# Kernel optimization log

Hardware: AMD Instinct MI355X
Metric: run time of the kernel (lower is better)

The kernel has to match this reference:

```python
import jax, jax.numpy as jnp
import numpy as np

B, H, W, C = 8, 128, 128, 256
NH = 8
HD = C // NH
WS = 8           # window size
SS = 4           # shift size
N = WS * WS      # tokens per window
SCALE = HD ** -0.5
EPS = 1e-5


def _rel_pos_index():
    coords = np.stack(np.meshgrid(np.arange(WS), np.arange(WS), indexing='ij'))  # [2,WS,WS]
    cf = coords.reshape(2, -1)                                                   # [2,N]
    rel = (cf[:, :, None] - cf[:, None, :]).transpose(1, 2, 0)                   # [N,N,2]
    rel[..., 0] += WS - 1
    rel[..., 1] += WS - 1
    rel[..., 0] *= 2 * WS - 1
    return rel.sum(-1)  # [N,N] indices into (2*WS-1)^2 table

RPI = jnp.asarray(_rel_pos_index())


def _attn_mask():
    img = np.zeros((H, W))
    slices = (slice(0, -WS), slice(-WS, -SS), slice(-SS, None))
    cnt = 0
    for hs in slices:
        for ws_ in slices:
            img[hs, ws_] = cnt
            cnt += 1
    mw = img.reshape(H // WS, WS, W // WS, WS).transpose(0, 2, 1, 3).reshape(-1, N)  # [nW,N]
    am = mw[:, None, :] - mw[:, :, None]
    return jnp.asarray(np.where(am != 0, -100.0, 0.0).astype(np.float32))  # [nW,N,N]

ATTN_MASK = _attn_mask()


def _ln(x, g, b):
    m = jnp.mean(x, -1, keepdims=True)
    v = jnp.var(x, -1, keepdims=True)
    return (x - m) * jax.lax.rsqrt(v + EPS) * g + b


def setup_inputs() -> dict:
    key = jax.random.key(0)
    ks = jax.random.split(key, 8)
    s = 0.02
    return {
        'x': jax.random.normal(ks[0], (B, H * W, C), jnp.float32),
        'qkv_w': jax.random.normal(ks[1], (C, 3 * C), jnp.float32) * s,
        'qkv_b': jnp.zeros((3 * C,), jnp.float32),
        'proj_w': jax.random.normal(ks[2], (C, C), jnp.float32) * s,
        'proj_b': jnp.zeros((C,), jnp.float32),
        'rpb': jax.random.normal(ks[3], ((2 * WS - 1) ** 2, NH), jnp.float32) * s,
        'g1': jnp.ones((C,), jnp.float32), 'b1': jnp.zeros((C,), jnp.float32),
        'g2': jnp.ones((C,), jnp.float32), 'b2': jnp.zeros((C,), jnp.float32),
        'fc1_w': jax.random.normal(ks[4], (C, 4 * C), jnp.float32) * s,
        'fc1_b': jnp.zeros((4 * C,), jnp.float32),
        'fc2_w': jax.random.normal(ks[5], (4 * C, C), jnp.float32) * s,
        'fc2_b': jnp.zeros((C,), jnp.float32),
    }


def reference(x, qkv_w, qkv_b, proj_w, proj_b, rpb, g1, b1, g2, b2,
              fc1_w, fc1_b, fc2_w, fc2_b):
    nW = (H // WS) * (W // WS)
    shortcut = x
    h = _ln(x, g1, b1).reshape(B, H, W, C)
    # cyclic shift
    h = jnp.roll(h, (-SS, -SS), axis=(1, 2))
    # window partition -> (B*nW, N, C)
    win = h.reshape(B, H // WS, WS, W // WS, WS, C).transpose(0, 1, 3, 2, 4, 5).reshape(-1, N, C)
    qkv = (win @ qkv_w + qkv_b).reshape(-1, N, 3, NH, HD).transpose(2, 0, 3, 1, 4)  # [3,B_,NH,N,HD]
    q, k, v = qkv[0] * SCALE, qkv[1], qkv[2]
    attn = jnp.einsum('bhnd,bhmd->bhnm', q, k)                    # [B_,NH,N,N]
    bias = rpb[RPI].transpose(2, 0, 1)                             # [NH,N,N]
    attn = attn + bias[None]
    attn = attn.reshape(B, nW, NH, N, N) + ATTN_MASK[None, :, None]
    attn = jax.nn.softmax(attn.reshape(-1, NH, N, N), axis=-1)
    out = jnp.einsum('bhnm,bhmd->bhnd', attn, v).transpose(0, 2, 1, 3).reshape(-1, N, C)
    out = out @ proj_w + proj_b
    # window reverse + reverse shift
    out = out.reshape(B, H // WS, W // WS, WS, WS, C).transpose(0, 1, 3, 2, 4, 5).reshape(B, H, W, C)
    out = jnp.roll(out, (SS, SS), axis=(1, 2)).reshape(B, H * W, C)
    x = shortcut + out
    hm = _ln(x, g2, b2)
    hm = jax.nn.gelu(hm @ fc1_w + fc1_b, approximate=False) @ fc2_w + fc2_b
    return x + hm
```

## Files before the change

kernel.cpp:

```cpp
#include <hip/hip_runtime.h>
#include <math.h>


#define NWIN_TOTAL 2048
#define TOK_TOTAL  131072
#define SCALE_Q    0.17677669529663687f
#define LOG2E      1.4426950408889634f

typedef unsigned short u16;
typedef __attribute__((ext_vector_type(4))) unsigned short u16x4;
typedef __attribute__((ext_vector_type(8))) unsigned short u16x8;
typedef __attribute__((ext_vector_type(8))) short bf16x8;
typedef __attribute__((ext_vector_type(4))) float f32x4;

#define AS1 __attribute__((address_space(1)))
#define AS3 __attribute__((address_space(3)))
#define GLOAD_LDS16(g, l) \
  __builtin_amdgcn_global_load_lds((const AS1 unsigned int*)(g), (AS3 unsigned int*)(l), 16, 0, 0)

__device__ __forceinline__ float bf2f(u16 u) {
  union { unsigned int i; float f; } c; c.i = ((unsigned int)u) << 16; return c.f;
}
__device__ __forceinline__ u16 f2bf(float f) {
  union { float f; unsigned int i; } c; c.f = f;
  return (u16)((c.i + 0x7fff + ((c.i >> 16) & 1)) >> 16);
}
__device__ __forceinline__ int regid3(int h) { return h < 120 ? 0 : (h < 124 ? 1 : 2); }
__device__ __forceinline__ float gelu_f(float v) {
  float t = exp2f(v * fmaf(v * v, 0.10294423f, 2.3022082f));
  return v * t * __builtin_amdgcn_rcpf(t + 1.0f);
}

__device__ __forceinline__ int win_tok_to_t(int g, int n) {
  int b = g >> 8, wi = g & 255;
  int wr = wi >> 4, wc = wi & 15;
  int hs = wr * 8 + (n >> 3), ws2 = wc * 8 + (n & 7);
  int h = (hs + 4) & 127, w = (ws2 + 4) & 127;
  return (b << 14) + (h << 7) + w;
}

__global__ __launch_bounds__(256)
void wconv_kernel(const float* __restrict__ w, u16* __restrict__ wt, int K, int N)
{
  int i = blockIdx.x * 256 + threadIdx.x;
  if (i >= K * N) return;
  int k = i / N, n = i - k * N;
  wt[(size_t)n * K + k] = f2bf(w[i]);
}

__global__ __launch_bounds__(256)
void ln1_kernel(const float* __restrict__ x, const float* __restrict__ g1,
                const float* __restrict__ b1, u16* __restrict__ outw, int g0)
{
  int gid  = blockIdx.x * 4 + (threadIdx.x >> 6);
  int lane = threadIdx.x & 63;
  int g = g0 + (gid >> 6);
  int t = win_tok_to_t(g, gid & 63);
  float4 v = ((const float4*)x)[(size_t)t * 64 + lane];
  float s = v.x + v.y + v.z + v.w;
  float q = v.x * v.x + v.y * v.y + v.z * v.z + v.w * v.w;
#pragma unroll
  for (int m = 1; m < 64; m <<= 1) { s += __shfl_xor(s, m, 64); q += __shfl_xor(q, m, 64); }
  float mean = s * 0.00390625f;
  float var  = q * 0.00390625f - mean * mean;
  float rstd = rsqrtf(var + 1e-5f);
  float4 gg = ((const float4*)g1)[lane];
  float4 bb = ((const float4*)b1)[lane];
  u16x4 o;
  o.x = f2bf((v.x - mean) * rstd * gg.x + bb.x);
  o.y = f2bf((v.y - mean) * rstd * gg.y + bb.y);
  o.z = f2bf((v.z - mean) * rstd * gg.z + bb.z);
  o.w = f2bf((v.w - mean) * rstd * gg.w + bb.w);
  *(u16x4*)(outw + (size_t)gid * 256 + lane * 4) = o;
}

struct BArgs {
  const u16* A; const u16* Bt; const float* bias;
  u16* q; u16* k; u16* v;
  int M, N, K;
};

__global__ __launch_bounds__(256)
void qkv_gemm(BArgs a)
{
  __shared__ u16 As[2][4096];
  __shared__ u16 Bs[2][4096];
  const int tid  = threadIdx.x;
  const int wid  = tid >> 6, lane = tid & 63;
  const int wr   = wid >> 1, wc = wid & 1;
  const int gx = gridDim.x;
  const int nwg = gx * gridDim.y;
  const int p = blockIdx.y * gx + blockIdx.x;
  const int qq = nwg >> 3, rr = nwg & 7, xcd = p & 7;
  const int l = (xcd < rr ? xcd * (qq + 1) : rr * (qq + 1) + (xcd - rr) * qq) + (p >> 3);
  const int rowBase = (l / gx) * 128;
  const int colBase = (l % gx) * 128;
  const int lr = lane >> 2;
  const int lc = (lane & 3) * 8;
  const int l15 = lane & 15, lhi = lane >> 4;

  f32x4 acc[4][4];
#pragma unroll
  for (int m = 0; m < 4; ++m)
#pragma unroll
    for (int n = 0; n < 4; ++n) acc[m][n] = (f32x4){0.f, 0.f, 0.f, 0.f};

  const int nkt = a.K >> 5;

#define STAGE(buf, kk)                                                          \
  {                                                                             \
    _Pragma("unroll")                                                           \
    for (int i = 0; i < 2; ++i) {                                               \
      const int srow = wid * 32 + i * 16;                                       \
      GLOAD_LDS16(a.A  + (size_t)(rowBase + srow + lr) * a.K + (kk) + lc,       \
                  &As[buf][srow * 32]);                                         \
      GLOAD_LDS16(a.Bt + (size_t)(colBase + srow + lr) * a.K + (kk) + lc,       \
                  &Bs[buf][srow * 32]);                                         \
    }                                                                           \
  }

  STAGE(0, 0);
  __syncthreads();
  int cur = 0;
  for (int kt = 0; kt < nkt; ++kt) {
    if (kt + 1 < nkt) STAGE(cur ^ 1, (kt + 1) << 5);
    bf16x8 af[4], bfr[4];
#pragma unroll
    for (int m = 0; m < 4; ++m)
      af[m] = *(const bf16x8*)&As[cur][(wr * 64 + m * 16 + l15) * 32 + lhi * 8];
#pragma unroll
    for (int n = 0; n < 4; ++n)
      bfr[n] = *(const bf16x8*)&Bs[cur][(wc * 64 + n * 16 + l15) * 32 + lhi * 8];
#pragma unroll
    for (int m = 0; m < 4; ++m)
#pragma unroll
      for (int n = 0; n < 4; ++n)
        acc[m][n] = __builtin_amdgcn_mfma_f32_16x16x32_bf16(af[m], bfr[n], acc[m][n], 0, 0, 0);
    __syncthreads();
    cur ^= 1;
  }
#undef STAGE

#pragma unroll
  for (int n = 0; n < 4; ++n) {
    const int col16 = colBase + wc * 64 + n * 16;
    const float bv = a.bias[col16 + l15];
    u16* qdst = nullptr; float scl = 1.f; size_t obase = 0;
    int vsel = 0;
    {
      const int s = col16 >> 8, head = (col16 >> 5) & 7, hd = col16 & 31;
      if (s == 2) {
        vsel = 1;
        obase = ((size_t)head << 11) + (size_t)(hd + l15) * 64;
      } else {
        qdst = (s == 0) ? a.q : a.k;
        if (s == 0) scl = SCALE_Q * LOG2E;
        obase = ((size_t)head << 11) + hd + l15;
      }
    }
#pragma unroll
    for (int m = 0; m < 4; ++m) {
      const int row0 = rowBase + wr * 64 + m * 16 + lhi * 4;
      if (vsel) {
        const int gw = row0 >> 6, tok0 = row0 & 63;
        u16x4 pk;
#pragma unroll
        for (int r = 0; r < 4; ++r) pk[r] = f2bf(acc[m][n][r] + bv);
        *(u16x4*)&a.v[((size_t)gw << 14) + obase + tok0] = pk;
        continue;
      }
#pragma unroll
      for (int r = 0; r < 4; ++r) {
        const int row = row0 + r;
        const int gw = row >> 6, tok = row & 63;
        qdst[((size_t)gw << 14) + obase + ((size_t)tok << 5)] = f2bf((acc[m][n][r] + bv) * scl);
      }
    }
  }
}

__global__ __launch_bounds__(512)
void awp_kernel(const u16* __restrict__ qb, const u16* __restrict__ kb,
                const u16* __restrict__ vt, const float* __restrict__ rpb,
                const u16* __restrict__ pjT, const float* __restrict__ pjb,
                const float* __restrict__ x, float* __restrict__ out, int g0)
{
  __shared__ union {
    u16 pl[8][2048];
    u16 aoL[16384];
    float rep[8192];
  } sb;
  __shared__ float rl[1800];
  const int tid = threadIdx.x, hh = tid >> 6, lane = tid & 63;
  const int l15 = lane & 15, g = lane >> 4;
  const int bw = blockIdx.x;

  for (int i = tid; i < 1800; i += 512) {
    unsigned int h2 = (unsigned)i / 225u;
    unsigned int rem = (unsigned)i - h2 * 225u;
    unsigned int aa = rem / 15u, bb = rem - aa * 15u;
    rl[i] = rpb[(aa * 15u + 14u - bb) * 8u + h2] * LOG2E;
  }
  __syncthreads();

  const size_t base = ((size_t)(bw * 8 + hh)) << 11;

  bf16x8 qf[4], kf[4];
#pragma unroll
  for (int f = 0; f < 4; ++f) {
    qf[f] = *(const bf16x8*)(qb + base + (size_t)(f * 16 + l15) * 32 + g * 8);
    kf[f] = *(const bf16x8*)(kb + base + (size_t)(f * 16 + l15) * 32 + g * 8);
  }
  f32x4 acc[4][4];
#pragma unroll
  for (int mf = 0; mf < 4; ++mf)
#pragma unroll
    for (int nf = 0; nf < 4; ++nf) acc[mf][nf] = (f32x4){0.f, 0.f, 0.f, 0.f};
#pragma unroll
  for (int mf = 0; mf < 4; ++mf)
#pragma unroll
    for (int nf = 0; nf < 4; ++nf)
      acc[mf][nf] = __builtin_amdgcn_mfma_f32_16x16x32_bf16(kf[mf], qf[nf], acc[mf][nf], 0, 0, 0);

  const int gwin = g0 + bw;
  const int wrw = (gwin >> 4) & 15, wcw = gwin & 15;
  const bool edge = (wrw == 15) || (wcw == 15);
  const int i2b = g >> 1;
  const int j2b = (g & 1) * 4;
#pragma unroll
  for (int nf = 0; nf < 4; ++nf) {
    const int n = nf * 16 + l15;
    const int i1 = n >> 3, j1 = n & 7;
    const int rid1 = edge ? regid3(wrw * 8 + i1) * 3 + regid3(wcw * 8 + j1) : 0;
#pragma unroll
    for (int mf = 0; mf < 4; ++mf) {
      const int i2 = mf * 2 + i2b;
      const int ib = hh * 225 + (i1 - i2 + 7) * 15 + (j2b - j1 + 7);
      const int r2a = edge ? regid3(wrw * 8 + i2) * 3 : 0;
#pragma unroll
      for (int r = 0; r < 4; ++r) {
        float b = rl[ib + r];
        if (edge) {
          int rid2 = r2a + regid3(wcw * 8 + j2b + r);
          if (rid2 != rid1) b -= 144.2695f;
        }
        acc[mf][nf][r] += b;
      }
    }
  }

  float inv[4];
#pragma unroll
  for (int nf = 0; nf < 4; ++nf) {
    float m0 = -1e30f;
#pragma unroll
    for (int mf = 0; mf < 4; ++mf)
#pragma unroll
      for (int r = 0; r < 4; ++r) m0 = fmaxf(m0, acc[mf][nf][r]);
    m0 = fmaxf(m0, __shfl_xor(m0, 16, 64));
    m0 = fmaxf(m0, __shfl_xor(m0, 32, 64));
    float s = 0.f;
#pragma unroll
    for (int mf = 0; mf < 4; ++mf)
#pragma unroll
      for (int r = 0; r < 4; ++r) {
        float p = exp2f(acc[mf][nf][r] - m0);
        acc[mf][nf][r] = p;
        s += p;
      }
    s += __shfl_xor(s, 16, 64);
    s += __shfl_xor(s, 32, 64);
    inv[nf] = 1.f / s;
  }

  bf16x8 vf[2][2];
#pragma unroll
  for (int df = 0; df < 2; ++df)
#pragma unroll
    for (int ks = 0; ks < 2; ++ks)
      vf[df][ks] = *(const bf16x8*)(vt + base + (size_t)(df * 16 + l15) * 64 + ks * 32 + g * 8);
  f32x4 accO[4][2];
#pragma unroll
  for (int nf = 0; nf < 4; ++nf)
#pragma unroll
    for (int df = 0; df < 2; ++df) accO[nf][df] = (f32x4){0.f, 0.f, 0.f, 0.f};
  char* plw = (char*)sb.pl[hh];
#pragma unroll
  for (int ks = 0; ks < 2; ++ks) {
#pragma unroll
    for (int nf = 0; nf < 4; ++nf) {
      const int n = nf * 16 + l15;
      const int swz = (n & 3) << 4;
#pragma unroll
      for (int mm = 0; mm < 2; ++mm) {
        const int mf = ks * 2 + mm;
        float p0 = acc[mf][nf][0] * inv[nf], p1 = acc[mf][nf][1] * inv[nf];
        float p2 = acc[mf][nf][2] * inv[nf], p3 = acc[mf][nf][3] * inv[nf];
        unsigned int pa, pb;
        asm("v_cvt_pk_bf16_f32 %0, %1, %2" : "=v"(pa) : "v"(p0), "v"(p1));
        asm("v_cvt_pk_bf16_f32 %0, %1, %2" : "=v"(pb) : "v"(p2), "v"(p3));
        uint2 w; w.x = pa; w.y = pb;
        *(uint2*)(plw + ((n * 64 + mm * 32 + g * 8) ^ swz)) = w;
      }
    }
#pragma unroll
    for (int nf = 0; nf < 4; ++nf) {
      const int n = nf * 16 + l15;
      const int swz = (n & 3) << 4;
      bf16x8 pf = *(const bf16x8*)(plw + ((n * 64 + g * 16) ^ swz));
#pragma unroll
      for (int df = 0; df < 2; ++df)
        accO[nf][df] = __builtin_amdgcn_mfma_f32_16x16x32_bf16(pf, vf[df][ks], accO[nf][df], 0, 0, 0);
    }
  }

  __syncthreads();
#pragma unroll
  for (int nf = 0; nf < 4; ++nf)
#pragma unroll
    for (int r = 0; r < 4; ++r) {
      const int tok = nf * 16 + g * 4 + r;
#pragma unroll
      for (int df = 0; df < 2; ++df) {
        const int ch = hh * 32 + df * 16 + l15;
        *(u16*)((char*)sb.aoL + tok * 512 + ((((ch >> 3) ^ (tok & 7))) << 4) + (ch & 7) * 2) =
            f2bf(accO[nf][df][r]);
      }
    }
  __syncthreads();

  f32x4 pacc[4][2];
#pragma unroll
  for (int mf = 0; mf < 4; ++mf)
#pragma unroll
    for (int of = 0; of < 2; ++of) pacc[mf][of] = (f32x4){0.f, 0.f, 0.f, 0.f};
  const u16* pB = pjT + (size_t)(hh * 32) * 256;
#pragma unroll
  for (int ks = 0; ks < 8; ++ks) {
    bf16x8 af[4], bwf[2];
#pragma unroll
    for (int mf = 0; mf < 4; ++mf) {
      const int tok = mf * 16 + l15;
      af[mf] = *(const bf16x8*)((char*)sb.aoL + tok * 512 + (((ks * 4 + g) ^ (tok & 7)) << 4));
    }
#pragma unroll
    for (int of = 0; of < 2; ++of)
      bwf[of] = *(const bf16x8*)(pB + (size_t)(of * 16 + l15) * 256 + ks * 32 + g * 8);
#pragma unroll
    for (int mf = 0; mf < 4; ++mf)
#pragma unroll
      for (int of = 0; of < 2; ++of)
        pacc[mf][of] = __builtin_amdgcn_mfma_f32_16x16x32_bf16(af[mf], bwf[of], pacc[mf][of], 0, 0, 0);
  }

#pragma unroll
  for (int hp = 0; hp < 2; ++hp) {
    __syncthreads();
#pragma unroll
    for (int mm = 0; mm < 2; ++mm) {
      const int mf = hp * 2 + mm;
#pragma unroll
      for (int of = 0; of < 2; ++of) {
        const int oc = hh * 32 + of * 16 + l15;
        const float bv = pjb[oc];
#pragma unroll
        for (int r = 0; r < 4; ++r) {
          const int row = mm * 16 + g * 4 + r;
          *(float*)((char*)sb.rep + ((row * 1024 + oc * 4) ^ ((row & 3) << 4))) =
              pacc[mf][of][r] + bv;
        }
      }
    }
    __syncthreads();
    const int rowl = tid >> 4, coll = (tid & 15) * 16;
    const int tok = hp * 32 + rowl;
    const int t = win_tok_to_t(g0 + bw, tok);
    const float* xs = x + (size_t)t * 256 + coll;
    float* od = out + (size_t)t * 256 + coll;
#pragma unroll
    for (int i = 0; i < 4; ++i) {
      float4 rv = *(const float4*)((char*)sb.rep +
                    ((rowl * 1024 + (coll + i * 4) * 4) ^ ((rowl & 3) << 4)));
      float4 xv = ((const float4*)xs)[i];
      ((float4*)od)[i] = make_float4(rv.x + xv.x, rv.y + xv.y, rv.z + xv.z, rv.w + xv.w);
    }
  }
}

__global__ __launch_bounds__(512)
void mlp_kernel(float* io, const u16* __restrict__ w1t, const u16* __restrict__ w2t,
                const float* __restrict__ fb1, const float* __restrict__ fb2,
                const float* __restrict__ g2, const float* __restrict__ bt2)
{
  __shared__ u16 Aln[16384];
  __shared__ u16 Hs[8192];
  const int tid = threadIdx.x, wid = tid >> 6, lane = tid & 63;
  const int l15 = lane & 15, g = lane >> 4;
  const int t0 = blockIdx.x * 64;

  {
    const int row = tid >> 3;
    const int cq = (tid & 7) * 32;
    const float* src = io + (size_t)(t0 + row) * 256 + cq;
    float vals[32];
    float s = 0.f, q = 0.f;
#pragma unroll
    for (int i = 0; i < 8; ++i) {
      float4 v = ((const float4*)src)[i];
      vals[i*4] = v.x; vals[i*4+1] = v.y; vals[i*4+2] = v.z; vals[i*4+3] = v.w;
      s += v.x + v.y + v.z + v.w;
      q += v.x*v.x + v.y*v.y + v.z*v.z + v.w*v.w;
    }
    s += __shfl_xor(s, 1, 64); q += __shfl_xor(q, 1, 64);
    s += __shfl_xor(s, 2, 64); q += __shfl_xor(q, 2, 64);
    s += __shfl_xor(s, 4, 64); q += __shfl_xor(q, 4, 64);
    float mean = s * 0.00390625f;
    float rstd = rsqrtf(q * 0.00390625f - mean * mean + 1e-5f);
#pragma unroll
    for (int i = 0; i < 4; ++i) {
      const int col = cq + i * 8;
      u16x8 o;
#pragma unroll
      for (int j = 0; j < 8; ++j)
        o[j] = f2bf((vals[i*8+j] - mean) * rstd * g2[col+j] + bt2[col+j]);
      const int gran = col >> 3;
      *(u16x8*)((char*)Aln + row * 512 + ((gran ^ (row & 7)) << 4)) = o;
    }
  }
  __syncthreads();

  f32x4 acc2[4][2];
#pragma unroll
  for (int m = 0; m < 4; ++m)
#pragma unroll
    for (int n = 0; n < 2; ++n) acc2[m][n] = (f32x4){0.f, 0.f, 0.f, 0.f};

  for (int c = 0; c < 8; ++c) {
    f32x4 acc1[4];
#pragma unroll
    for (int tf = 0; tf < 4; ++tf) acc1[tf] = (f32x4){0.f, 0.f, 0.f, 0.f};
    const u16* w1base = w1t + (size_t)(c * 128 + wid * 16) * 256;
#pragma unroll
    for (int ks = 0; ks < 8; ++ks) {
      bf16x8 af = *(const bf16x8*)(w1base + (size_t)l15 * 256 + ks * 32 + g * 8);
      bf16x8 bfr[4];
#pragma unroll
      for (int tf = 0; tf < 4; ++tf) {
        const int tok = tf * 16 + l15;
        const int gran = ks * 4 + g;
        bfr[tf] = *(const bf16x8*)&Aln[tok * 256 + ((gran ^ (tok & 7)) << 3)];
      }
#pragma unroll
      for (int tf = 0; tf < 4; ++tf)
        acc1[tf] = __builtin_amdgcn_mfma_f32_16x16x32_bf16(af, bfr[tf], acc1[tf], 0, 0, 0);
    }
    __syncthreads();
    {
      const int hcl = wid * 16 + g * 4;
      const float b0 = fb1[c * 128 + hcl];
      const float b1 = fb1[c * 128 + hcl + 1];
      const float b2v = fb1[c * 128 + hcl + 2];
      const float b3 = fb1[c * 128 + hcl + 3];
#pragma unroll
      for (int tf = 0; tf < 4; ++tf) {
        const int tok = tf * 16 + l15;
        float p0 = gelu_f(acc1[tf][0] + b0);
        float p1 = gelu_f(acc1[tf][1] + b1);
        float p2 = gelu_f(acc1[tf][2] + b2v);
        float p3 = gelu_f(acc1[tf][3] + b3);
        unsigned int pa, pb;
        asm("v_cvt_pk_bf16_f32 %0, %1, %2" : "=v"(pa) : "v"(p0), "v"(p1));
        asm("v_cvt_pk_bf16_f32 %0, %1, %2" : "=v"(pb) : "v"(p2), "v"(p3));
        uint2 w; w.x = pa; w.y = pb;
        *(uint2*)((char*)Hs + tok * 256 + (((hcl >> 3) ^ (tok & 7)) << 4) + ((hcl & 4) << 1)) = w;
      }
    }
    __syncthreads();
    const u16* w2base = w2t + (size_t)(wid * 32) * 1024 + c * 128;
#pragma unroll
    for (int hk = 0; hk < 4; ++hk) {
      bf16x8 ah[4], bw[2];
#pragma unroll
      for (int tf = 0; tf < 4; ++tf) {
        const int tok = tf * 16 + l15;
        const int gran = hk * 4 + g;
        ah[tf] = *(const bf16x8*)&Hs[tok * 128 + ((gran ^ (tok & 7)) << 3)];
      }
#pragma unroll
      for (int of = 0; of < 2; ++of)
        bw[of] = *(const bf16x8*)(w2base + (size_t)(of * 16 + l15) * 1024 + hk * 32 + g * 8);
#pragma unroll
      for (int tf = 0; tf < 4; ++tf)
#pragma unroll
        for (int of = 0; of < 2; ++of)
          acc2[tf][of] = __builtin_amdgcn_mfma_f32_16x16x32_bf16(ah[tf], bw[of], acc2[tf][of], 0, 0, 0);
    }
  }

#pragma unroll
  for (int tf = 0; tf < 4; ++tf) {
#pragma unroll
    for (int of = 0; of < 2; ++of) {
      const int oc = wid * 32 + of * 16 + l15;
      const float bv = fb2[oc];
#pragma unroll
      for (int r = 0; r < 4; ++r) {
        const size_t off = (size_t)(t0 + tf * 16 + g * 4 + r) * 256 + oc;
        io[off] = acc2[tf][of][r] + bv + io[off];
      }
    }
  }
}

extern "C" void kernel_launch(void* const* d_in, const int* in_sizes, int n_in,
                              void* d_out, int out_size, void* d_ws, size_t ws_size,
                              hipStream_t stream)
{
  const float* x      = (const float*)d_in[0];
  const float* qkv_w  = (const float*)d_in[1];
  const float* qkv_b  = (const float*)d_in[2];
  const float* proj_w = (const float*)d_in[3];
  const float* proj_b = (const float*)d_in[4];
  const float* rpb    = (const float*)d_in[5];
  const float* g1     = (const float*)d_in[6];
  const float* b1     = (const float*)d_in[7];
  const float* g2     = (const float*)d_in[8];
  const float* b2     = (const float*)d_in[9];
  const float* fc1_w  = (const float*)d_in[10];
  const float* fc1_b  = (const float*)d_in[11];
  const float* fc2_w  = (const float*)d_in[12];
  const float* fc2_b  = (const float*)d_in[13];
  float* out = (float*)d_out;
  char* ws = (char*)d_ws;

  u16* qkvT  = (u16*)ws;
  u16* projT = qkvT + 196608;
  u16* fc1T  = projT + 65536;
  u16* fc2T  = fc1T + 262144;
  char* pb = (char*)(fc2T + 262144);
  size_t used = 1572864ULL;
  size_t R = ws_size > used ? ws_size - used : 0;

  wconv_kernel<<<(196608 + 255) / 256, 256, 0, stream>>>(qkv_w, qkvT, 256, 768);
  wconv_kernel<<<(65536  + 255) / 256, 256, 0, stream>>>(proj_w, projT, 256, 256);
  wconv_kernel<<<(262144 + 255) / 256, 256, 0, stream>>>(fc1_w, fc1T, 256, 1024);
  wconv_kernel<<<(262144 + 255) / 256, 256, 0, stream>>>(fc2_w, fc2T, 1024, 256);

  int Gc = 2048;
  while (Gc > 2 && (size_t)Gc * 131072ULL > R) Gc >>= 1;

  u16* ln1w = (u16*)pb;
  u16* qb = ln1w + (size_t)Gc * 16384;
  u16* kb = qb + (size_t)Gc * 16384;
  u16* vb = kb + (size_t)Gc * 16384;

  for (int g0 = 0; g0 < NWIN_TOTAL; g0 += Gc) {
    int nT = Gc * 64;
    ln1_kernel<<<nT / 4, 256, 0, stream>>>(x, g1, b1, ln1w, g0);

    BArgs qa = {}; qa.A = ln1w; qa.Bt = qkvT; qa.bias = qkv_b;
    qa.q = qb; qa.k = kb; qa.v = vb; qa.M = nT; qa.N = 768; qa.K = 256;
    qkv_gemm<<<dim3(6, nT / 128), 256, 0, stream>>>(qa);

    awp_kernel<<<Gc, 512, 0, stream>>>(qb, kb, vb, rpb, projT, proj_b, x, out, g0);
  }

  mlp_kernel<<<TOK_TOTAL / 64, 512, 0, stream>>>(out, fc1T, fc2T, fc1_b, fc2_b, g2, b2);
}
```

Measured before the change: 655.2 us.

## Fuse LayerNorm1 into per-window QKV projection kernel

Replaces the separate LN1 kernel and the tiled QKV GEMM with one kernel per window. Each 1024-thread block normalizes its 64 tokens into XOR-swizzled LDS, then 16 waves each compute 48 output columns, reading weight fragments straight from global memory. This drops the bf16 LN1 intermediate buffer round trip and one kernel launch. The cost is that the QKV weights are re-read from global/L2 by every window block with no LDS staging or double buffering, and the per-block GEMM tile is smaller.

```diff
diff --git a/kernel.cpp b/kernel.cpp
--- a/kernel.cpp
+++ b/kernel.cpp
@@ -48,133 +48,103 @@
   wt[(size_t)n * K + k] = f2bf(w[i]);
 }
 
-__global__ __launch_bounds__(256)
-void ln1_kernel(const float* __restrict__ x, const float* __restrict__ g1,
-                const float* __restrict__ b1, u16* __restrict__ outw, int g0)
+__global__ __launch_bounds__(1024)
+void qln_kernel(const float* __restrict__ x, const float* __restrict__ g1,
+                const float* __restrict__ b1, const u16* __restrict__ qkvT,
+                const float* __restrict__ qkv_b,
+                u16* __restrict__ qb, u16* __restrict__ kb, u16* __restrict__ vb,
+                int g0)
 {
-  int gid  = blockIdx.x * 4 + (threadIdx.x >> 6);
-  int lane = threadIdx.x & 63;
-  int g = g0 + (gid >> 6);
-  int t = win_tok_to_t(g, gid & 63);
-  float4 v = ((const float4*)x)[(size_t)t * 64 + lane];
-  float s = v.x + v.y + v.z + v.w;
-  float q = v.x * v.x + v.y * v.y + v.z * v.z + v.w * v.w;
-#pragma unroll
-  for (int m = 1; m < 64; m <<= 1) { s += __shfl_xor(s, m, 64); q += __shfl_xor(q, m, 64); }
-  float mean = s * 0.00390625f;
-  float var  = q * 0.00390625f - mean * mean;
-  float rstd = rsqrtf(var + 1e-5f);
-  float4 gg = ((const float4*)g1)[lane];
-  float4 bb = ((const float4*)b1)[lane];
-  u16x4 o;
-  o.x = f2bf((v.x - mean) * rstd * gg.x + bb.x);
-  o.y = f2bf((v.y - mean) * rstd * gg.y + bb.y);
-  o.z = f2bf((v.z - mean) * rstd * gg.z + bb.z);
-  o.w = f2bf((v.w - mean) * rstd * gg.w + bb.w);
-  *(u16x4*)(outw + (size_t)gid * 256 + lane * 4) = o;
-}
-
-struct BArgs {
-  const u16* A; const u16* Bt; const float* bias;
-  u16* q; u16* k; u16* v;
-  int M, N, K;
-};
-
-__global__ __launch_bounds__(256)
-void qkv_gemm(BArgs a)
-{
-  __shared__ u16 As[2][4096];
-  __shared__ u16 Bs[2][4096];
-  const int tid  = threadIdx.x;
-  const int wid  = tid >> 6, lane = tid & 63;
-  const int wr   = wid >> 1, wc = wid & 1;
-  const int gx = gridDim.x;
-  const int nwg = gx * gridDim.y;
-  const int p = blockIdx.y * gx + blockIdx.x;
-  const int qq = nwg >> 3, rr = nwg & 7, xcd = p & 7;
-  const int l = (xcd < rr ? xcd * (qq + 1) : rr * (qq + 1) + (xcd - rr) * qq) + (p >> 3);
-  const int rowBase = (l / gx) * 128;
-  const int colBase = (l % gx) * 128;
-  const int lr = lane >> 2;
-  const int lc = (lane & 3) * 8;
-  const int l15 = lane & 15, lhi = lane >> 4;
-
-  f32x4 acc[4][4];
+  __shared__ u16 Aln[16384];
+  const int tid = threadIdx.x, wid = tid >> 6, lane = tid & 63;
+  const int l15 = lane & 15, g = lane >> 4;
+  const int bwi = blockIdx.x;
+  const int gw = g0 + bwi;
+
+  {
+    const int row = tid >> 4;
+    const int cq = (tid & 15) * 16;
+    const int t = win_tok_to_t(gw, row);
+    const float* src = x + (size_t)t * 256 + cq;
+    float vals[16];
+    float s = 0.f, q = 0.f;
+#pragma unroll
+    for (int i = 0; i < 4; ++i) {
+      float4 v = ((const float4*)src)[i];
+      vals[i*4] = v.x; vals[i*4+1] = v.y; vals[i*4+2] = v.z; vals[i*4+3] = v.w;
+      s += v.x + v.y + v.z + v.w;
+      q += v.x*v.x + v.y*v.y + v.z*v.z + v.w*v.w;
+    }
+    s += __shfl_xor(s, 1, 64); q += __shfl_xor(q, 1, 64);
+    s += __shfl_xor(s, 2, 64); q += __shfl_xor(q, 2, 64);
+    s += __shfl_xor(s, 4, 64); q += __shfl_xor(q, 4, 64);
+    s += __shfl_xor(s, 8, 64); q += __shfl_xor(q, 8, 64);
+    float mean = s * 0.00390625f;
+    float rstd = rsqrtf(q * 0.00390625f - mean * mean + 1e-5f);
+#pragma unroll
+    for (int i = 0; i < 2; ++i) {
+      const int col = cq + i * 8;
+      u16x8 o;
+#pragma unroll
+      for (int j = 0; j < 8; ++j)
+        o[j] = f2bf((vals[i*8+j] - mean) * rstd * g1[col+j] + b1[col+j]);
+      const int gran = col >> 3;
+      *(u16x8*)((char*)Aln + row * 512 + ((gran ^ (row & 7)) << 4)) = o;
+    }
+  }
+  __syncthreads();
+
+  f32x4 acc[4][3];
 #pragma unroll
   for (int m = 0; m < 4; ++m)
 #pragma unroll
-    for (int n = 0; n < 4; ++n) acc[m][n] = (f32x4){0.f, 0.f, 0.f, 0.f};
-
-  const int nkt = a.K >> 5;
-
-#define STAGE(buf, kk)                                                          \
-  {                                                                             \
-    _Pragma("unroll")                                                           \
-    for (int i = 0; i < 2; ++i) {                                               \
-      const int srow = wid * 32 + i * 16;                                       \
-      GLOAD_LDS16(a.A  + (size_t)(rowBase + srow + lr) * a.K + (kk) + lc,       \
-                  &As[buf][srow * 32]);                                         \
-      GLOAD_LDS16(a.Bt + (size_t)(colBase + srow + lr) * a.K + (kk) + lc,       \
-                  &Bs[buf][srow * 32]);                                         \
-    }                                                                           \
-  }
-
-  STAGE(0, 0);
-  __syncthreads();
-  int cur = 0;
-  for (int kt = 0; kt < nkt; ++kt) {
-    if (kt + 1 < nkt) STAGE(cur ^ 1, (kt + 1) << 5);
-    bf16x8 af[4], bfr[4];
+    for (int n = 0; n < 3; ++n) acc[m][n] = (f32x4){0.f, 0.f, 0.f, 0.f};
+  const int colb = wid * 48;
+#pragma unroll
+  for (int ks = 0; ks < 8; ++ks) {
+    bf16x8 af[4], bw[3];
+#pragma unroll
+    for (int m = 0; m < 4; ++m) {
+      const int tok = m * 16 + l15;
+      const int gran = ks * 4 + g;
+      af[m] = *(const bf16x8*)&Aln[tok * 256 + ((gran ^ (tok & 7)) << 3)];
+    }
+#pragma unroll
+    for (int n = 0; n < 3; ++n)
+      bw[n] = *(const bf16x8*)(qkvT + (size_t)(colb + n * 16 + l15) * 256 + ks * 32 + g * 8);
 #pragma unroll
     for (int m = 0; m < 4; ++m)
-      af[m] = *(const bf16x8*)&As[cur][(wr * 64 + m * 16 + l15) * 32 + lhi * 8];
-#pragma unroll
-    for (int n = 0; n < 4; ++n)
-      bfr[n] = *(const bf16x8*)&Bs[cur][(wc * 64 + n * 16 + l15) * 32 + lhi * 8];
-#pragma unroll
-    for (int m = 0; m < 4; ++m)
-#pragma unroll
-      for (int n = 0; n < 4; ++n)
-        acc[m][n] = __builtin_amdgcn_mfma_f32_16x16x32_bf16(af[m], bfr[n], acc[m][n], 0, 0, 0);
-    __syncthreads();
-    cur ^= 1;
-  }
-#undef STAGE
-
-#pragma unroll
-  for (int n = 0; n < 4; ++n) {
-    const int col16 = colBase + wc * 64 + n * 16;
-    const float bv = a.bias[col16 + l15];
-    u16* qdst = nullptr; float scl = 1.f; size_t obase = 0;
-    int vsel = 0;
-    {
-      const int s = col16 >> 8, head = (col16 >> 5) & 7, hd = col16 & 31;
-      if (s == 2) {
-        vsel = 1;
-        obase = ((size_t)head << 11) + (size_t)(hd + l15) * 64;
-      } else {
-        qdst = (s == 0) ? a.q : a.k;
-        if (s == 0) scl = SCALE_Q * LOG2E;
-        obase = ((size_t)head << 11) + hd + l15;
-      }
-    }
-#pragma unroll
-    for (int m = 0; m < 4; ++m) {
-      const int row0 = rowBase + wr * 64 + m * 16 + lhi * 4;
-      if (vsel) {
-        const int gw = row0 >> 6, tok0 = row0 & 63;
+#pragma unroll
+      for (int n = 0; n < 3; ++n)
+        acc[m][n] = __builtin_amdgcn_mfma_f32_16x16x32_bf16(af[m], bw[n], acc[m][n], 0, 0, 0);
+  }
+
+#pragma unroll
+  for (int n = 0; n < 3; ++n) {
+    const int col16 = colb + n * 16;
+    const float bv = qkv_b[col16 + l15];
+    const int s = col16 >> 8, head = (col16 >> 5) & 7, hd = col16 & 31;
+    if (s == 2) {
+      const size_t obase = ((size_t)bwi << 14) + ((size_t)head << 11) + (size_t)(hd + l15) * 64;
+#pragma unroll
+      for (int m = 0; m < 4; ++m) {
+        const int tok0 = m * 16 + g * 4;
         u16x4 pk;
 #pragma unroll
         for (int r = 0; r < 4; ++r) pk[r] = f2bf(acc[m][n][r] + bv);
-        *(u16x4*)&a.v[((size_t)gw << 14) + obase + tok0] = pk;
-        continue;
-      }
-#pragma unroll
-      for (int r = 0; r < 4; ++r) {
-        const int row = row0 + r;
-        const int gw = row >> 6, tok = row & 63;
-        qdst[((size_t)gw << 14) + obase + ((size_t)tok << 5)] = f2bf((acc[m][n][r] + bv) * scl);
-      }
+        *(u16x4*)&vb[obase + tok0] = pk;
+      }
+    } else {
+      u16* qdst = (s == 0) ? qb : kb;
+      const float scl = (s == 0) ? SCALE_Q * LOG2E : 1.f;
+      const size_t obase = ((size_t)bwi << 14) + ((size_t)head << 11) + hd + l15;
+#pragma unroll
+      for (int m = 0; m < 4; ++m)
+#pragma unroll
+        for (int r = 0; r < 4; ++r) {
+          const int tok = m * 16 + g * 4 + r;
+          qdst[obase + ((size_t)tok << 5)] = f2bf((acc[m][n][r] + bv) * scl);
+        }
     }
   }
 }
@@ -547,21 +517,14 @@
   wconv_kernel<<<(262144 + 255) / 256, 256, 0, stream>>>(fc2_w, fc2T, 1024, 256);
 
   int Gc = 2048;
-  while (Gc > 2 && (size_t)Gc * 131072ULL > R) Gc >>= 1;
-
-  u16* ln1w = (u16*)pb;
-  u16* qb = ln1w + (size_t)Gc * 16384;
+  while (Gc > 2 && (size_t)Gc * 98304ULL > R) Gc >>= 1;
+
+  u16* qb = (u16*)pb;
   u16* kb = qb + (size_t)Gc * 16384;
   u16* vb = kb + (size_t)Gc * 16384;
 
   for (int g0 = 0; g0 < NWIN_TOTAL; g0 += Gc) {
-    int nT = Gc * 64;
-    ln1_kernel<<<nT / 4, 256, 0, stream>>>(x, g1, b1, ln1w, g0);
-
-    BArgs qa = {}; qa.A = ln1w; qa.Bt = qkvT; qa.bias = qkv_b;
-    qa.q = qb; qa.k = kb; qa.v = vb; qa.M = nT; qa.N = 768; qa.K = 256;
-    qkv_gemm<<<dim3(6, nT / 128), 256, 0, stream>>>(qa);
-
+    qln_kernel<<<Gc, 1024, 0, stream>>>(x, g1, b1, qkvT, qkv_b, qb, kb, vb, g0);
     awp_kernel<<<Gc, 512, 0, stream>>>(qb, kb, vb, rpb, projT, proj_b, x, out, g0);
   }
 
```

New measurement: 651.6 us. No clear change (-0.6%).
